# Performance work log

Measured on AMD Instinct MI355X. Metric: run time of the kernel, lower is better.

## Reference

```python
import jax, jax.numpy as jnp
import numpy as np

NB_NODE = 100000
FT = 256
OUT_FT = 256
NB_REL = 4
BATCH = 8192
DEG = 16  # padded neighbors per (node, relation)


def setup_inputs() -> dict:
    key = jax.random.key(0)
    k1, k2, k3, k4 = jax.random.split(key, 4)
    features = jax.random.normal(k1, (NB_NODE, FT), dtype=jnp.float32)
    neighbor_idx = jax.random.randint(k2, (BATCH, NB_REL, DEG), 0, NB_NODE, dtype=jnp.int32)
    # per-relation GCN weight, scaled like xavier
    W = jax.random.normal(k3, (NB_REL, FT, OUT_FT), dtype=jnp.float32) * (1.0 / np.sqrt(FT))
    b = jnp.zeros((NB_REL, OUT_FT), dtype=jnp.float32)
    prelu_a = jnp.full((1,), 0.25, dtype=jnp.float32)  # nn.PReLU() default single param
    node_list = jax.random.randint(k4, (BATCH,), 0, NB_NODE, dtype=jnp.int32)
    return {"features": features, "neighbor_idx": neighbor_idx, "W": W, "b": b,
            "prelu_a": prelu_a, "node_list": node_list, "k": 0}


def _prelu(x, a):
    return jnp.where(x >= 0, x, a * x)


def reference(features, neighbor_idx, W, b, prelu_a, node_list, k):
    # Ragged per-relation neighbor gather + mean (vectorized form of the
    # python double loop): [B, R, D, F] -> mean over D -> [B, R, F]
    v_in = jnp.mean(features[neighbor_idx], axis=2)
    # Per-relation GCN linear + PReLU: [B, R, F] x [R, F, O] -> [B, R, O]
    h = jnp.einsum('brf,rfo->bro', v_in, W) + b[None, :, :]
    h = _prelu(h, prelu_a[0])
    # isAtt=False branch: mean over relations -> [B, O]
    return jnp.mean(h, axis=1)
```

## Files before the change

### kernel.cpp

```cpp
#include <hip/hip_runtime.h>
#include <hip/hip_bf16.h>

#define B_TOT 8192
#define FT    256
#define NREL  4
#define DEG   16

typedef __attribute__((ext_vector_type(8))) short bf16x8;
typedef __attribute__((ext_vector_type(4))) float f32x4;

static __device__ __forceinline__ unsigned short f2bf(float x) {
    union { float f; unsigned int u; } c; c.f = x;
    unsigned int u = c.u;
    u += 0x7fffu + ((u >> 16) & 1u);
    return (unsigned short)(u >> 16);
}
static __device__ __forceinline__ float bf2f(unsigned short h) {
    union { unsigned int u; float f; } c; c.u = ((unsigned int)h) << 16;
    return c.f;
}

__global__ __launch_bounds__(256) void cvt_feat_k(const float* __restrict__ f,
                                                  unsigned short* __restrict__ fb,
                                                  int n4) {
    int i = blockIdx.x * 256 + threadIdx.x;
    if (i < n4) {
        float4 x = ((const float4*)f)[i];
        ushort4 o;
        o.x = f2bf(x.x); o.y = f2bf(x.y); o.z = f2bf(x.z); o.w = f2bf(x.w);
        ((ushort4*)fb)[i] = o;
    }
}

__global__ __launch_bounds__(256) void wtrans_k(const float* __restrict__ W,
                                                unsigned short* __restrict__ Wt) {
    __shared__ float t[64][65];
    int r = blockIdx.z, ft = blockIdx.y, ot = blockIdx.x;
    int c = threadIdx.x & 63, rw = threadIdx.x >> 6;
    const float* src = W + ((size_t)r * 256 + ft * 64) * 256 + ot * 64;
#pragma unroll
    for (int i = 0; i < 16; ++i) {
        int row = i * 4 + rw;
        t[row][c] = src[(size_t)row * 256 + c];
    }
    __syncthreads();
    unsigned short* dst = Wt + ((size_t)r * 256 + ot * 64) * 256 + ft * 64;
#pragma unroll
    for (int i = 0; i < 16; ++i) {
        int row = i * 4 + rw;
        dst[(size_t)row * 256 + c] = f2bf(t[c][row]);
    }
}

__global__ __launch_bounds__(256) void gather_mean_bf16_k(const unsigned short* __restrict__ fb,
                                                          const int* __restrict__ nidx,
                                                          unsigned short* __restrict__ v) {
    int wave = threadIdx.x >> 6;
    int lane = threadIdx.x & 63;
    int task = blockIdx.x * 4 + wave;
    int b = task >> 2, r = task & 3;
    const int* idx = nidx + ((size_t)b * NREL + r) * DEG;
    int4 i0 = *(const int4*)(idx);
    int4 i1 = *(const int4*)(idx + 4);
    int4 i2 = *(const int4*)(idx + 8);
    int4 i3 = *(const int4*)(idx + 12);
    float s0 = 0.f, s1 = 0.f, s2 = 0.f, s3 = 0.f;
#define ACC(nn) { const ushort4 x = ((const ushort4*)(fb + (size_t)(nn) * FT))[lane]; \
                  s0 += bf2f(x.x); s1 += bf2f(x.y); s2 += bf2f(x.z); s3 += bf2f(x.w); }
    ACC(i0.x) ACC(i0.y) ACC(i0.z) ACC(i0.w)
    ACC(i1.x) ACC(i1.y) ACC(i1.z) ACC(i1.w)
    ACC(i2.x) ACC(i2.y) ACC(i2.z) ACC(i2.w)
    ACC(i3.x) ACC(i3.y) ACC(i3.z) ACC(i3.w)
#undef ACC
    const float inv = 1.0f / 16.0f;
    ushort4 o;
    o.x = f2bf(s0 * inv); o.y = f2bf(s1 * inv);
    o.z = f2bf(s2 * inv); o.w = f2bf(s3 * inv);
    *(ushort4*)(v + ((size_t)r * B_TOT + b) * FT + 4 * lane) = o;
}

__global__ __launch_bounds__(256) void gather_mean_k(const float* __restrict__ feat,
                                                     const int* __restrict__ nidx,
                                                     unsigned short* __restrict__ v) {
    int wave = threadIdx.x >> 6;
    int lane = threadIdx.x & 63;
    int task = blockIdx.x * 4 + wave;
    int b = task >> 2, r = task & 3;
    const int* idx = nidx + ((size_t)b * NREL + r) * DEG;
    int4 i0 = *(const int4*)(idx);
    int4 i1 = *(const int4*)(idx + 4);
    int4 i2 = *(const int4*)(idx + 8);
    int4 i3 = *(const int4*)(idx + 12);
    float4 s = make_float4(0.f, 0.f, 0.f, 0.f);
#define ACC(nn) { const float4 x = ((const float4*)(feat + (size_t)(nn) * FT))[lane]; \
                  s.x += x.x; s.y += x.y; s.z += x.z; s.w += x.w; }
    ACC(i0.x) ACC(i0.y) ACC(i0.z) ACC(i0.w)
    ACC(i1.x) ACC(i1.y) ACC(i1.z) ACC(i1.w)
    ACC(i2.x) ACC(i2.y) ACC(i2.z) ACC(i2.w)
    ACC(i3.x) ACC(i3.y) ACC(i3.z) ACC(i3.w)
#undef ACC
    const float inv = 1.0f / 16.0f;
    ushort4 o;
    o.x = f2bf(s.x * inv); o.y = f2bf(s.y * inv);
    o.z = f2bf(s.z * inv); o.w = f2bf(s.w * inv);
    *(ushort4*)(v + ((size_t)r * B_TOT + b) * FT + 4 * lane) = o;
}

__global__ __launch_bounds__(256) void gemm_k(const unsigned short* __restrict__ v,
                                              const unsigned short* __restrict__ Wt,
                                              const float* __restrict__ bias,
                                              const float* __restrict__ prelu,
                                              float* __restrict__ out) {
    __shared__ unsigned short As[64][264];
    __shared__ unsigned short Bs[64][264];
    int tid  = threadIdx.x;
    int lane = tid & 63, w = tid >> 6;
    int wm = w >> 1, wn = w & 1;
    int mrow = lane & 15, quad = lane >> 4;
    int m0 = blockIdx.x * 64, n0 = blockIdx.y * 64;
    float pa = prelu[0];

    f32x4 accO[2][2] = {};
    int ocol0 = n0 + wn * 32 + mrow;

    for (int r = 0; r < NREL; ++r) {
        const unsigned short* Ag = v  + ((size_t)r * B_TOT + m0) * FT;
        const unsigned short* Bg = Wt + ((size_t)r * 256  + n0) * FT;
#pragma unroll
        for (int i = 0; i < 8; ++i) {
            int u = tid + i * 256;
            int row = u >> 5, c8 = (u & 31) * 8;
            *(int4*)(&As[row][c8]) = *(const int4*)(Ag + row * FT + c8);
            *(int4*)(&Bs[row][c8]) = *(const int4*)(Bg + row * FT + c8);
        }
        __syncthreads();

        f32x4 acc[2][2] = {};
#pragma unroll
        for (int kk = 0; kk < 8; ++kk) {
            int k0 = kk * 32 + quad * 8;
            bf16x8 a0 = *(const bf16x8*)&As[wm * 32 + mrow][k0];
            bf16x8 a1 = *(const bf16x8*)&As[wm * 32 + 16 + mrow][k0];
            bf16x8 b0 = *(const bf16x8*)&Bs[wn * 32 + mrow][k0];
            bf16x8 b1 = *(const bf16x8*)&Bs[wn * 32 + 16 + mrow][k0];
            acc[0][0] = __builtin_amdgcn_mfma_f32_16x16x32_bf16(a0, b0, acc[0][0], 0, 0, 0);
            acc[1][0] = __builtin_amdgcn_mfma_f32_16x16x32_bf16(a1, b0, acc[1][0], 0, 0, 0);
            acc[0][1] = __builtin_amdgcn_mfma_f32_16x16x32_bf16(a0, b1, acc[0][1], 0, 0, 0);
            acc[1][1] = __builtin_amdgcn_mfma_f32_16x16x32_bf16(a1, b1, acc[1][1], 0, 0, 0);
        }
        __syncthreads();

        float b0v = bias[r * 256 + ocol0];
        float b1v = bias[r * 256 + ocol0 + 16];
#pragma unroll
        for (int mt = 0; mt < 2; ++mt)
#pragma unroll
            for (int i = 0; i < 4; ++i) {
                float h0 = acc[mt][0][i] + b0v; h0 = (h0 >= 0.f) ? h0 : pa * h0;
                float h1 = acc[mt][1][i] + b1v; h1 = (h1 >= 0.f) ? h1 : pa * h1;
                accO[mt][0][i] += h0;
                accO[mt][1][i] += h1;
            }
    }

#pragma unroll
    for (int mt = 0; mt < 2; ++mt)
#pragma unroll
        for (int i = 0; i < 4; ++i) {
            int row = m0 + wm * 32 + mt * 16 + quad * 4 + i;
            out[(size_t)row * 256 + ocol0]      = accO[mt][0][i] * 0.25f;
            out[(size_t)row * 256 + ocol0 + 16] = accO[mt][1][i] * 0.25f;
        }
}

extern "C" void kernel_launch(void* const* d_in, const int* in_sizes, int n_in,
                              void* d_out, int out_size, void* d_ws, size_t ws_size,
                              hipStream_t stream) {
    const float* feat  = (const float*)d_in[0];
    const int*   nidx  = (const int*)  d_in[1];
    const float* W     = (const float*)d_in[2];
    const float* bias  = (const float*)d_in[3];
    const float* prelu = (const float*)d_in[4];
    float* out = (float*)d_out;

    const size_t feat_elems = (size_t)in_sizes[0];
    const size_t fb_bytes = feat_elems * 2;
    const size_t v_bytes  = (size_t)NREL * B_TOT * FT * 2;
    const size_t wt_bytes = (size_t)NREL * 256 * FT * 2;

    if (ws_size >= fb_bytes + v_bytes + wt_bytes) {
        unsigned short* fb = (unsigned short*)d_ws;
        unsigned short* v  = fb + feat_elems;
        unsigned short* Wt = v + (size_t)NREL * B_TOT * FT;
        int n4 = (int)(feat_elems / 4);
        cvt_feat_k<<<(n4 + 255) / 256, 256, 0, stream>>>(feat, fb, n4);
        wtrans_k<<<dim3(4, 4, 4), 256, 0, stream>>>(W, Wt);
        gather_mean_bf16_k<<<B_TOT, 256, 0, stream>>>(fb, nidx, v);
        gemm_k<<<dim3(B_TOT / 64, 256 / 64), 256, 0, stream>>>(v, Wt, bias, prelu, out);
    } else {
        unsigned short* v  = (unsigned short*)d_ws;
        unsigned short* Wt = v + (size_t)NREL * B_TOT * FT;
        wtrans_k<<<dim3(4, 4, 4), 256, 0, stream>>>(W, Wt);
        gather_mean_k<<<B_TOT, 256, 0, stream>>>(feat, nidx, v);
        gemm_k<<<dim3(B_TOT / 64, 256 / 64), 256, 0, stream>>>(v, Wt, bias, prelu, out);
    }
}
```

Measured before the change: 215.1 us.

## Fuse neighbor gather-mean with per-relation GEMM and PReLU into one kernel

Merges the gather/mean kernel and the GEMM kernel into a single kernel. Each block handles 16 batch rows: it stages the neighbor indices in shared memory, builds the bf16 mean features for each relation in LDS, then runs MFMA against W read directly from global memory. This removes the intermediate v buffer write/read and one launch. The cost is a small M tile with B operands fetched from global/L2 without LDS reuse, plus only 512 blocks.

```diff
diff --git a/kernel.cpp b/kernel.cpp
--- a/kernel.cpp
+++ b/kernel.cpp
@@ -1,10 +1,10 @@
 #include <hip/hip_runtime.h>
-#include <hip/hip_bf16.h>
 
 #define B_TOT 8192
 #define FT    256
 #define NREL  4
 #define DEG   16
+#define BM    16
 
 typedef __attribute__((ext_vector_type(8))) short bf16x8;
 typedef __attribute__((ext_vector_type(4))) float f32x4;
@@ -52,125 +52,101 @@
     }
 }
 
-__global__ __launch_bounds__(256) void gather_mean_bf16_k(const unsigned short* __restrict__ fb,
-                                                          const int* __restrict__ nidx,
-                                                          unsigned short* __restrict__ v) {
-    int wave = threadIdx.x >> 6;
-    int lane = threadIdx.x & 63;
-    int task = blockIdx.x * 4 + wave;
-    int b = task >> 2, r = task & 3;
-    const int* idx = nidx + ((size_t)b * NREL + r) * DEG;
-    int4 i0 = *(const int4*)(idx);
-    int4 i1 = *(const int4*)(idx + 4);
-    int4 i2 = *(const int4*)(idx + 8);
-    int4 i3 = *(const int4*)(idx + 12);
-    float s0 = 0.f, s1 = 0.f, s2 = 0.f, s3 = 0.f;
+template <bool BF16TAB>
+__global__ __launch_bounds__(256) void fused_k(const void* __restrict__ ftab_,
+                                               const int* __restrict__ nidx,
+                                               const unsigned short* __restrict__ Wt,
+                                               const float* __restrict__ bias,
+                                               const float* __restrict__ prelu,
+                                               float* __restrict__ out) {
+    __shared__ int shIdx[BM * NREL * DEG];
+    __shared__ unsigned short As[BM][FT + 8];
+    const int tid  = threadIdx.x;
+    const int lane = tid & 63, w = tid >> 6;
+    const int blk  = blockIdx.x;
+    const int mrow = lane & 15, quad = lane >> 4;
+    const float pa = prelu[0];
+
+    ((int4*)shIdx)[tid] = ((const int4*)(nidx + (size_t)blk * BM * NREL * DEG))[tid];
+    __syncthreads();
+
+    const int ncol = w * 64 + mrow;
+    f32x4 accO[4] = {};
+
+    for (int r = 0; r < NREL; ++r) {
+#pragma unroll
+        for (int j = 0; j < 4; ++j) {
+            const int m = w * 4 + j;
+            const int* ip = shIdx + (m * NREL + r) * DEG;
+            const int4 i0 = *(const int4*)(ip);
+            const int4 i1 = *(const int4*)(ip + 4);
+            const int4 i2 = *(const int4*)(ip + 8);
+            const int4 i3 = *(const int4*)(ip + 12);
+            float s0 = 0.f, s1 = 0.f, s2 = 0.f, s3 = 0.f;
+            if constexpr (BF16TAB) {
+                const unsigned short* fb = (const unsigned short*)ftab_;
 #define ACC(nn) { const ushort4 x = ((const ushort4*)(fb + (size_t)(nn) * FT))[lane]; \
                   s0 += bf2f(x.x); s1 += bf2f(x.y); s2 += bf2f(x.z); s3 += bf2f(x.w); }
-    ACC(i0.x) ACC(i0.y) ACC(i0.z) ACC(i0.w)
-    ACC(i1.x) ACC(i1.y) ACC(i1.z) ACC(i1.w)
-    ACC(i2.x) ACC(i2.y) ACC(i2.z) ACC(i2.w)
-    ACC(i3.x) ACC(i3.y) ACC(i3.z) ACC(i3.w)
+                ACC(i0.x) ACC(i0.y) ACC(i0.z) ACC(i0.w)
+                ACC(i1.x) ACC(i1.y) ACC(i1.z) ACC(i1.w)
+                ACC(i2.x) ACC(i2.y) ACC(i2.z) ACC(i2.w)
+                ACC(i3.x) ACC(i3.y) ACC(i3.z) ACC(i3.w)
 #undef ACC
-    const float inv = 1.0f / 16.0f;
-    ushort4 o;
-    o.x = f2bf(s0 * inv); o.y = f2bf(s1 * inv);
-    o.z = f2bf(s2 * inv); o.w = f2bf(s3 * inv);
-    *(ushort4*)(v + ((size_t)r * B_TOT + b) * FT + 4 * lane) = o;
-}
-
-__global__ __launch_bounds__(256) void gather_mean_k(const float* __restrict__ feat,
-                                                     const int* __restrict__ nidx,
-                                                     unsigned short* __restrict__ v) {
-    int wave = threadIdx.x >> 6;
-    int lane = threadIdx.x & 63;
-    int task = blockIdx.x * 4 + wave;
-    int b = task >> 2, r = task & 3;
-    const int* idx = nidx + ((size_t)b * NREL + r) * DEG;
-    int4 i0 = *(const int4*)(idx);
-    int4 i1 = *(const int4*)(idx + 4);
-    int4 i2 = *(const int4*)(idx + 8);
-    int4 i3 = *(const int4*)(idx + 12);
-    float4 s = make_float4(0.f, 0.f, 0.f, 0.f);
-#define ACC(nn) { const float4 x = ((const float4*)(feat + (size_t)(nn) * FT))[lane]; \
-                  s.x += x.x; s.y += x.y; s.z += x.z; s.w += x.w; }
-    ACC(i0.x) ACC(i0.y) ACC(i0.z) ACC(i0.w)
-    ACC(i1.x) ACC(i1.y) ACC(i1.z) ACC(i1.w)
-    ACC(i2.x) ACC(i2.y) ACC(i2.z) ACC(i2.w)
-    ACC(i3.x) ACC(i3.y) ACC(i3.z) ACC(i3.w)
+            } else {
+                const float* ff = (const float*)ftab_;
+#define ACC(nn) { const float4 x = ((const float4*)(ff + (size_t)(nn) * FT))[lane]; \
+                  s0 += x.x; s1 += x.y; s2 += x.z; s3 += x.w; }
+                ACC(i0.x) ACC(i0.y) ACC(i0.z) ACC(i0.w)
+                ACC(i1.x) ACC(i1.y) ACC(i1.z) ACC(i1.w)
+                ACC(i2.x) ACC(i2.y) ACC(i2.z) ACC(i2.w)
+                ACC(i3.x) ACC(i3.y) ACC(i3.z) ACC(i3.w)
 #undef ACC
-    const float inv = 1.0f / 16.0f;
-    ushort4 o;
-    o.x = f2bf(s.x * inv); o.y = f2bf(s.y * inv);
-    o.z = f2bf(s.z * inv); o.w = f2bf(s.w * inv);
-    *(ushort4*)(v + ((size_t)r * B_TOT + b) * FT + 4 * lane) = o;
-}
-
-__global__ __launch_bounds__(256) void gemm_k(const unsigned short* __restrict__ v,
-                                              const unsigned short* __restrict__ Wt,
-                                              const float* __restrict__ bias,
-                                              const float* __restrict__ prelu,
-                                              float* __restrict__ out) {
-    __shared__ unsigned short As[64][264];
-    __shared__ unsigned short Bs[64][264];
-    int tid  = threadIdx.x;
-    int lane = tid & 63, w = tid >> 6;
-    int wm = w >> 1, wn = w & 1;
-    int mrow = lane & 15, quad = lane >> 4;
-    int m0 = blockIdx.x * 64, n0 = blockIdx.y * 64;
-    float pa = prelu[0];
-
-    f32x4 accO[2][2] = {};
-    int ocol0 = n0 + wn * 32 + mrow;
-
-    for (int r = 0; r < NREL; ++r) {
-        const unsigned short* Ag = v  + ((size_t)r * B_TOT + m0) * FT;
-        const unsigned short* Bg = Wt + ((size_t)r * 256  + n0) * FT;
-#pragma unroll
-        for (int i = 0; i < 8; ++i) {
-            int u = tid + i * 256;
-            int row = u >> 5, c8 = (u & 31) * 8;
-            *(int4*)(&As[row][c8]) = *(const int4*)(Ag + row * FT + c8);
-            *(int4*)(&Bs[row][c8]) = *(const int4*)(Bg + row * FT + c8);
+            }
+            const float inv = 1.0f / 16.0f;
+            ushort4 o;
+            o.x = f2bf(s0 * inv); o.y = f2bf(s1 * inv);
+            o.z = f2bf(s2 * inv); o.w = f2bf(s3 * inv);
+            *(ushort4*)(&As[m][lane * 4]) = o;
         }
         __syncthreads();
 
-        f32x4 acc[2][2] = {};
+        const unsigned short* bp = Wt + ((size_t)(r * 256 + ncol)) * FT;
+        float bv[4];
+#pragma unroll
+        for (int t = 0; t < 4; ++t) bv[t] = bias[r * 256 + ncol + t * 16];
+
+        f32x4 acc[4] = {};
 #pragma unroll
         for (int kk = 0; kk < 8; ++kk) {
-            int k0 = kk * 32 + quad * 8;
-            bf16x8 a0 = *(const bf16x8*)&As[wm * 32 + mrow][k0];
-            bf16x8 a1 = *(const bf16x8*)&As[wm * 32 + 16 + mrow][k0];
-            bf16x8 b0 = *(const bf16x8*)&Bs[wn * 32 + mrow][k0];
-            bf16x8 b1 = *(const bf16x8*)&Bs[wn * 32 + 16 + mrow][k0];
-            acc[0][0] = __builtin_amdgcn_mfma_f32_16x16x32_bf16(a0, b0, acc[0][0], 0, 0, 0);
-            acc[1][0] = __builtin_amdgcn_mfma_f32_16x16x32_bf16(a1, b0, acc[1][0], 0, 0, 0);
-            acc[0][1] = __builtin_amdgcn_mfma_f32_16x16x32_bf16(a0, b1, acc[0][1], 0, 0, 0);
-            acc[1][1] = __builtin_amdgcn_mfma_f32_16x16x32_bf16(a1, b1, acc[1][1], 0, 0, 0);
+            const int k0 = kk * 32 + quad * 8;
+            const bf16x8 a  = *(const bf16x8*)(&As[mrow][k0]);
+            const bf16x8 b0 = *(const bf16x8*)(bp + k0);
+            const bf16x8 b1 = *(const bf16x8*)(bp + 16 * FT + k0);
+            const bf16x8 b2 = *(const bf16x8*)(bp + 32 * FT + k0);
+            const bf16x8 b3 = *(const bf16x8*)(bp + 48 * FT + k0);
+            acc[0] = __builtin_amdgcn_mfma_f32_16x16x32_bf16(a, b0, acc[0], 0, 0, 0);
+            acc[1] = __builtin_amdgcn_mfma_f32_16x16x32_bf16(a, b1, acc[1], 0, 0, 0);
+            acc[2] = __builtin_amdgcn_mfma_f32_16x16x32_bf16(a, b2, acc[2], 0, 0, 0);
+            acc[3] = __builtin_amdgcn_mfma_f32_16x16x32_bf16(a, b3, acc[3], 0, 0, 0);
         }
         __syncthreads();
 
-        float b0v = bias[r * 256 + ocol0];
-        float b1v = bias[r * 256 + ocol0 + 16];
 #pragma unroll
-        for (int mt = 0; mt < 2; ++mt)
+        for (int t = 0; t < 4; ++t)
 #pragma unroll
             for (int i = 0; i < 4; ++i) {
-                float h0 = acc[mt][0][i] + b0v; h0 = (h0 >= 0.f) ? h0 : pa * h0;
-                float h1 = acc[mt][1][i] + b1v; h1 = (h1 >= 0.f) ? h1 : pa * h1;
-                accO[mt][0][i] += h0;
-                accO[mt][1][i] += h1;
+                float h = acc[t][i] + bv[t];
+                h = (h >= 0.f) ? h : pa * h;
+                accO[t][i] += h;
             }
     }
 
+    const size_t rbase = (size_t)(blk * BM + quad * 4) * 256;
 #pragma unroll
-    for (int mt = 0; mt < 2; ++mt)
+    for (int t = 0; t < 4; ++t)
 #pragma unroll
-        for (int i = 0; i < 4; ++i) {
-            int row = m0 + wm * 32 + mt * 16 + quad * 4 + i;
-            out[(size_t)row * 256 + ocol0]      = accO[mt][0][i] * 0.25f;
-            out[(size_t)row * 256 + ocol0 + 16] = accO[mt][1][i] * 0.25f;
-        }
+        for (int i = 0; i < 4; ++i)
+            out[rbase + (size_t)i * 256 + ncol + t * 16] = accO[t][i] * 0.25f;
 }
 
 extern "C" void kernel_launch(void* const* d_in, const int* in_sizes, int n_in,
@@ -185,23 +161,18 @@
 
     const size_t feat_elems = (size_t)in_sizes[0];
     const size_t fb_bytes = feat_elems * 2;
-    const size_t v_bytes  = (size_t)NREL * B_TOT * FT * 2;
     const size_t wt_bytes = (size_t)NREL * 256 * FT * 2;
 
-    if (ws_size >= fb_bytes + v_bytes + wt_bytes) {
+    if (ws_size >= fb_bytes + wt_bytes) {
         unsigned short* fb = (unsigned short*)d_ws;
-        unsigned short* v  = fb + feat_elems;
-        unsigned short* Wt = v + (size_t)NREL * B_TOT * FT;
+        unsigned short* Wt = fb + feat_elems;
         int n4 = (int)(feat_elems / 4);
         cvt_feat_k<<<(n4 + 255) / 256, 256, 0, stream>>>(feat, fb, n4);
         wtrans_k<<<dim3(4, 4, 4), 256, 0, stream>>>(W, Wt);
-        gather_mean_bf16_k<<<B_TOT, 256, 0, stream>>>(fb, nidx, v);
-        gemm_k<<<dim3(B_TOT / 64, 256 / 64), 256, 0, stream>>>(v, Wt, bias, prelu, out);
+        fused_k<true><<<B_TOT / BM, 256, 0, stream>>>(fb, nidx, Wt, bias, prelu, out);
     } else {
-        unsigned short* v  = (unsigned short*)d_ws;
-        unsigned short* Wt = v + (size_t)NREL * B_TOT * FT;
+        unsigned short* Wt = (unsigned short*)d_ws;
         wtrans_k<<<dim3(4, 4, 4), 256, 0, stream>>>(W, Wt);
-        gather_mean_k<<<B_TOT, 256, 0, stream>>>(feat, nidx, v);
-        gemm_k<<<dim3(B_TOT / 64, 256 / 64), 256, 0, stream>>>(v, Wt, bias, prelu, out);
+        fused_k<false><<<B_TOT / BM, 256, 0, stream>>>(feat, nidx, Wt, bias, prelu, out);
     }
 }
```

New measurement: 243.7 us. 13.3% more time.

## Restructure GEMM to full-N per block, reading weights directly from global memory

Applied to the files above, without the earlier changes.

The GEMM kernel now gives each block 32 rows and all 256 output columns, so each block reads its A slice once instead of four times across N tiles. Weight fragments are loaded straight from global memory (L2-resident) rather than staged in shared memory, which cuts LDS use and the per-relation B staging. The grid shrinks from 512 to 256 blocks, which may underfill the GPU's CUs. The direct global B loads may also add latency on the MFMA path.

```diff
diff --git a/kernel.cpp b/kernel.cpp
--- a/kernel.cpp
+++ b/kernel.cpp
@@ -1,5 +1,4 @@
 #include <hip/hip_runtime.h>
-#include <hip/hip_bf16.h>
 
 #define B_TOT 8192
 #define FT    256
@@ -106,70 +105,72 @@
     *(ushort4*)(v + ((size_t)r * B_TOT + b) * FT + 4 * lane) = o;
 }
 
-__global__ __launch_bounds__(256) void gemm_k(const unsigned short* __restrict__ v,
-                                              const unsigned short* __restrict__ Wt,
-                                              const float* __restrict__ bias,
-                                              const float* __restrict__ prelu,
-                                              float* __restrict__ out) {
-    __shared__ unsigned short As[64][264];
-    __shared__ unsigned short Bs[64][264];
-    int tid  = threadIdx.x;
-    int lane = tid & 63, w = tid >> 6;
-    int wm = w >> 1, wn = w & 1;
-    int mrow = lane & 15, quad = lane >> 4;
-    int m0 = blockIdx.x * 64, n0 = blockIdx.y * 64;
-    float pa = prelu[0];
-
-    f32x4 accO[2][2] = {};
-    int ocol0 = n0 + wn * 32 + mrow;
+__global__ __launch_bounds__(256) void gemm2_k(const unsigned short* __restrict__ v,
+                                               const unsigned short* __restrict__ Wt,
+                                               const float* __restrict__ bias,
+                                               const float* __restrict__ prelu,
+                                               float* __restrict__ out) {
+    __shared__ unsigned short As[32][264];
+    const int tid  = threadIdx.x;
+    const int lane = tid & 63, w = tid >> 6;
+    const int mrow = lane & 15, quad = lane >> 4;
+    const int m0   = blockIdx.x * 32;
+    const float pa = prelu[0];
+
+    f32x4 accO[2][4] = {};
+    int ncol[4];
+#pragma unroll
+    for (int nt = 0; nt < 4; ++nt) ncol[nt] = w * 64 + nt * 16 + mrow;
 
     for (int r = 0; r < NREL; ++r) {
-        const unsigned short* Ag = v  + ((size_t)r * B_TOT + m0) * FT;
-        const unsigned short* Bg = Wt + ((size_t)r * 256  + n0) * FT;
-#pragma unroll
-        for (int i = 0; i < 8; ++i) {
+        const unsigned short* Ag = v + ((size_t)r * B_TOT + m0) * FT;
+#pragma unroll
+        for (int i = 0; i < 4; ++i) {
             int u = tid + i * 256;
             int row = u >> 5, c8 = (u & 31) * 8;
-            *(int4*)(&As[row][c8]) = *(const int4*)(Ag + row * FT + c8);
-            *(int4*)(&Bs[row][c8]) = *(const int4*)(Bg + row * FT + c8);
+            *(int4*)(&As[row][c8]) = *(const int4*)(Ag + (size_t)row * FT + c8);
         }
         __syncthreads();
 
-        f32x4 acc[2][2] = {};
+        float bv[4];
+#pragma unroll
+        for (int nt = 0; nt < 4; ++nt) bv[nt] = bias[r * 256 + ncol[nt]];
+
+        f32x4 acc[2][4] = {};
 #pragma unroll
         for (int kk = 0; kk < 8; ++kk) {
-            int k0 = kk * 32 + quad * 8;
-            bf16x8 a0 = *(const bf16x8*)&As[wm * 32 + mrow][k0];
-            bf16x8 a1 = *(const bf16x8*)&As[wm * 32 + 16 + mrow][k0];
-            bf16x8 b0 = *(const bf16x8*)&Bs[wn * 32 + mrow][k0];
-            bf16x8 b1 = *(const bf16x8*)&Bs[wn * 32 + 16 + mrow][k0];
-            acc[0][0] = __builtin_amdgcn_mfma_f32_16x16x32_bf16(a0, b0, acc[0][0], 0, 0, 0);
-            acc[1][0] = __builtin_amdgcn_mfma_f32_16x16x32_bf16(a1, b0, acc[1][0], 0, 0, 0);
-            acc[0][1] = __builtin_amdgcn_mfma_f32_16x16x32_bf16(a0, b1, acc[0][1], 0, 0, 0);
-            acc[1][1] = __builtin_amdgcn_mfma_f32_16x16x32_bf16(a1, b1, acc[1][1], 0, 0, 0);
+            const int k0 = kk * 32 + quad * 8;
+            const bf16x8 a0 = *(const bf16x8*)(&As[mrow][k0]);
+            const bf16x8 a1 = *(const bf16x8*)(&As[16 + mrow][k0]);
+#pragma unroll
+            for (int nt = 0; nt < 4; ++nt) {
+                const bf16x8 b = *(const bf16x8*)(Wt + ((size_t)(r * 256 + ncol[nt])) * FT + k0);
+                acc[0][nt] = __builtin_amdgcn_mfma_f32_16x16x32_bf16(a0, b, acc[0][nt], 0, 0, 0);
+                acc[1][nt] = __builtin_amdgcn_mfma_f32_16x16x32_bf16(a1, b, acc[1][nt], 0, 0, 0);
+            }
         }
         __syncthreads();
 
-        float b0v = bias[r * 256 + ocol0];
-        float b1v = bias[r * 256 + ocol0 + 16];
 #pragma unroll
         for (int mt = 0; mt < 2; ++mt)
 #pragma unroll
-            for (int i = 0; i < 4; ++i) {
-                float h0 = acc[mt][0][i] + b0v; h0 = (h0 >= 0.f) ? h0 : pa * h0;
-                float h1 = acc[mt][1][i] + b1v; h1 = (h1 >= 0.f) ? h1 : pa * h1;
-                accO[mt][0][i] += h0;
-                accO[mt][1][i] += h1;
-            }
+            for (int nt = 0; nt < 4; ++nt)
+#pragma unroll
+                for (int i = 0; i < 4; ++i) {
+                    float h = acc[mt][nt][i] + bv[nt];
+                    h = (h >= 0.f) ? h : pa * h;
+                    accO[mt][nt][i] += h;
+                }
     }
 
 #pragma unroll
     for (int mt = 0; mt < 2; ++mt)
 #pragma unroll
         for (int i = 0; i < 4; ++i) {
-            int row = m0 + wm * 32 + mt * 16 + quad * 4 + i;
-            out[(size_t)row * 256 + ocol0]      = accO[mt][0][i] * 0.25f;
-            out[(size_t)row * 256 + ocol0 + 16] = accO[mt][1][i] * 0.25f;
+            const size_t row = (size_t)(m0 + mt * 16 + quad * 4 + i) * 256;
+#pragma unroll
+            for (int nt = 0; nt < 4; ++nt)
+                out[row + ncol[nt]] = accO[mt][nt][i] * 0.25f;
         }
 }
 
@@ -196,12 +197,12 @@
         cvt_feat_k<<<(n4 + 255) / 256, 256, 0, stream>>>(feat, fb, n4);
         wtrans_k<<<dim3(4, 4, 4), 256, 0, stream>>>(W, Wt);
         gather_mean_bf16_k<<<B_TOT, 256, 0, stream>>>(fb, nidx, v);
-        gemm_k<<<dim3(B_TOT / 64, 256 / 64), 256, 0, stream>>>(v, Wt, bias, prelu, out);
+        gemm2_k<<<256, 256, 0, stream>>>(v, Wt, bias, prelu, out);
     } else {
         unsigned short* v  = (unsigned short*)d_ws;
         unsigned short* Wt = v + (size_t)NREL * B_TOT * FT;
         wtrans_k<<<dim3(4, 4, 4), 256, 0, stream>>>(W, Wt);
         gather_mean_k<<<B_TOT, 256, 0, stream>>>(feat, nidx, v);
-        gemm_k<<<dim3(B_TOT / 64, 256 / 64), 256, 0, stream>>>(v, Wt, bias, prelu, out);
-    }
-}
+        gemm2_k<<<256, 256, 0, stream>>>(v, Wt, bias, prelu, out);
+    }
+}
```

Result: slower. 233.0 us (+8.4%).
